# Optimization experiments

Hardware: AMD Instinct MI355X
Metric: run time of the kernel (lower is better)

The kernel has to match this reference:

```python
import jax, jax.numpy as jnp
import numpy as np

EMBED_DIM = 2048
NUM_HEADS = 16
HEAD_DIM = EMBED_DIM // NUM_HEADS  # 128
D_K = 128
SCALE = 1.0 / float(np.sqrt(HEAD_DIM))
LAYER_DEPTH = 6 / 12  # amrpa_layer_idx / n_amrpa_layers
BATCH, SEQ = 2, 2048


def setup_inputs() -> dict:
    key = jax.random.key(0)
    ks = jax.random.split(key, 8)
    return {
        "hidden_states": jax.random.normal(ks[0], (BATCH, SEQ, EMBED_DIM), jnp.float32),
        "c_attn_w": jax.random.normal(ks[1], (EMBED_DIM, 3 * EMBED_DIM), jnp.float32) * 0.02,
        "c_attn_b": jax.random.normal(ks[2], (3 * EMBED_DIM,), jnp.float32) * 0.02,
        "c_proj_w": jax.random.normal(ks[3], (EMBED_DIM, EMBED_DIM), jnp.float32) * 0.02,
        "c_proj_b": jax.random.normal(ks[4], (EMBED_DIM,), jnp.float32) * 0.02,
        "cam_gate": jax.random.normal(ks[5], (D_K,), jnp.float32) * 0.1,
        "cam_w0": jax.random.normal(ks[6], (1,), jnp.float32),
        "cam_w1": jax.random.normal(ks[7], (1,), jnp.float32),
    }


def reference(hidden_states, c_attn_w, c_attn_b, c_proj_w, c_proj_b, cam_gate, cam_w0, cam_w1):
    # GPT2 Conv1D-style fused QKV projection: [B,S,3E]
    qkv = hidden_states @ c_attn_w + c_attn_b
    Q, K, V = jnp.split(qkv, 3, axis=2)  # each [B,S,E]
    # NOTE: faithful to source — attention over the FULL embed dim (no head split),
    # scaled by 1/sqrt(head_dim); causal mask is computed but never applied upstream.
    attn_scores = jnp.einsum('bse,bte->bst', Q, K) * SCALE  # [B,S,S]

    # CAM: sliced low-rank channels
    Q_cam, K_cam, V_cam = Q[:, :, :D_K], K[:, :, :D_K], V[:, :, :D_K]
    # base attention map computed under no_grad in the original
    base_A = jax.lax.stop_gradient(
        jax.nn.softmax(jnp.einsum('bsd,btd->bst', Q_cam, K_cam) * SCALE, axis=-1))
    layer_weight = jax.nn.sigmoid(cam_w0[0] + cam_w1[0] * LAYER_DEPTH)
    cam_ctx = jnp.einsum('bst,btd->bsd', base_A, V_cam)            # [B,S,d_k]
    cam_bias = jnp.einsum('bsd,btd->bst', jnp.tanh(cam_ctx * cam_gate), K_cam)
    cam_bias = cam_bias * (SCALE * layer_weight)                   # cam_mask is all-ones

    final_attn = jax.nn.softmax(attn_scores + cam_bias, axis=-1)
    context = jnp.einsum('bst,bte->bse', final_attn, V)            # [B,S,E]
    output = context @ c_proj_w + c_proj_b                         # resid_dropout is identity (eval)
    return output
```

## Files before the change

### kernel.cpp

```cpp
#include <hip/hip_runtime.h>
#include <hip/hip_bf16.h>

typedef unsigned short u16;
typedef __attribute__((ext_vector_type(8))) __bf16 bf16x8;
typedef __attribute__((ext_vector_type(4))) float f32x4;
typedef __attribute__((ext_vector_type(4))) unsigned short u16x4;

#define SCALE_QK 0.08838834764831845f

__device__ __forceinline__ u16 f2bf(float x) {
  union { float f; unsigned u; } v; v.f = x;
  unsigned r = v.u + 0x7fffu + ((v.u >> 16) & 1u);
  return (u16)(r >> 16);
}

__device__ __forceinline__ void gload_lds16(const u16* g, u16* l) {
  __builtin_amdgcn_global_load_lds(
      (const __attribute__((address_space(1))) unsigned*)g,
      (__attribute__((address_space(3))) unsigned*)l, 16, 0, 0);
}

#define CFENCE() asm volatile("" ::: "memory")
#define WAITV(N) asm volatile("s_waitcnt vmcnt(" #N ")" ::: "memory")

template<bool OUT_BF16, bool HAS_BIAS, bool TWO_SEG>
__global__ __launch_bounds__(512, 2)
void g128d(const u16* __restrict__ A1, int lda1, long sA1,
           const u16* __restrict__ B1, int ldb1, long sB1, int K1,
           const u16* __restrict__ A2, int lda2, long sA2,
           const u16* __restrict__ B2, int ldb2, long sB2, int K2,
           void* __restrict__ Cv, int ldc, long sC,
           float scale, const float* __restrict__ bias, int nbx)
{
  extern __shared__ u16 lds[];
  const int bz = blockIdx.z;
  const int nwg = gridDim.x, orig = blockIdx.x;
  const int q8 = nwg >> 3, r8 = nwg & 7;
  const int xcd = orig & 7, lp = orig >> 3;
  const int wg = (xcd < r8 ? xcd * (q8 + 1) : r8 * (q8 + 1) + (xcd - r8) * q8) + lp;
  const int bx = wg % nbx, by = wg / nbx;
  const long m0 = (long)by * 256, n0 = (long)bx * 128;

  const int tid = threadIdx.x, wid = tid >> 6, lane = tid & 63;
  const int wm = wid >> 1, wn = wid & 1;
  const int rl = lane & 15, g = lane >> 4;
  const int sw = ((g ^ ((rl >> 1) & 3)) << 3);

  int aoff[4], boff[4];
#pragma unroll
  for (int i = 0; i < 4; ++i) aoff[i] = (wm * 64 + i * 16 + rl) * 32 + sw;
#pragma unroll
  for (int j = 0; j < 4; ++j) boff[j] = (wn * 64 + j * 16 + rl) * 32 + sw;

  const int srow = tid >> 2;
  const int scolX = (((tid & 3) ^ ((srow >> 1) & 3)) << 3);

  f32x4 acc[4][4];
#pragma unroll
  for (int i = 0; i < 4; ++i)
#pragma unroll
    for (int j = 0; j < 4; ++j) acc[i][j] = (f32x4){0.f, 0.f, 0.f, 0.f};

  bf16x8 avA[4], bvA[4], avB[4], bvB[4];

#define STG6(H_, OA_) {                                                  \
    const u16* sa_ = Ab + (long)srow * lda + (H_) * 32 + scolX;          \
    u16* da_ = lds + (OA_) + tid * 8;                                    \
    gload_lds16(sa_, da_);                                               \
    gload_lds16(sa_ + (long)128 * lda, da_ + 4096);                      \
    gload_lds16(Bb + (long)srow * ldb + (H_) * 32 + scolX,               \
                lds + 49152 + ((OA_) >> 1) + tid * 8); }
#define RD6(OA_, AV, BV) {                                               \
    const u16* ap_ = lds + (OA_);                                        \
    const u16* bp_ = lds + 49152 + ((OA_) >> 1);                         \
    _Pragma("unroll") for (int i_ = 0; i_ < 4; ++i_)                     \
      AV[i_] = *(const bf16x8*)(ap_ + aoff[i_]);                         \
    _Pragma("unroll") for (int j_ = 0; j_ < 4; ++j_)                     \
      BV[j_] = *(const bf16x8*)(bp_ + boff[j_]); }
#define MMCL(CAV, CBV)                                                   \
    CFENCE(); __builtin_amdgcn_s_barrier();                              \
    asm volatile("s_waitcnt lgkmcnt(0)" ::: "memory");                   \
    __builtin_amdgcn_sched_barrier(0);                                   \
    __builtin_amdgcn_s_setprio(1);                                       \
    _Pragma("unroll") for (int i_ = 0; i_ < 4; ++i_)                     \
      _Pragma("unroll") for (int j_ = 0; j_ < 4; ++j_)                   \
        acc[i_][j_] = __builtin_amdgcn_mfma_f32_16x16x32_bf16(           \
            CAV[i_], CBV[j_], acc[i_][j_], 0, 0, 0);                     \
    __builtin_amdgcn_s_setprio(0);

  const int NSEG = TWO_SEG ? 2 : 1;
#pragma unroll 1
  for (int seg = 0; seg < NSEG; ++seg) {
    const int lda = (seg == 0) ? lda1 : lda2;
    const int ldb = (seg == 0) ? ldb1 : ldb2;
    const int K   = (seg == 0) ? K1 : K2;
    const u16* Ab = ((seg == 0) ? A1 + (long)bz * sA1 : A2 + (long)bz * sA2) + m0 * (long)lda;
    const u16* Bb = ((seg == 0) ? B1 + (long)bz * sB1 : B2 + (long)bz * sB2) + n0 * (long)ldb;
    const int NT = K >> 5;

    if (NT == 4) {
      STG6(0, 0); STG6(1, 8192); STG6(2, 16384); STG6(3, 24576);
      WAITV(9);
      CFENCE(); __builtin_amdgcn_s_barrier(); CFENCE();
      RD6(0, avA, bvA);
      CFENCE();
      WAITV(6); MMCL(avA, bvA); RD6(8192,  avB, bvB); CFENCE();
      WAITV(3); MMCL(avB, bvB); RD6(16384, avA, bvA); CFENCE();
      WAITV(0); MMCL(avA, bvA); RD6(24576, avB, bvB); CFENCE();
      MMCL(avB, bvB); CFENCE();
      __builtin_amdgcn_s_barrier();
      CFENCE();
    } else {
      STG6(0, 0); STG6(1, 8192); STG6(2, 16384); STG6(3, 24576); STG6(4, 32768);
      WAITV(12);
      CFENCE(); __builtin_amdgcn_s_barrier(); CFENCE();
      RD6(0, avA, bvA);
      STG6(5, 40960);
      CFENCE();

      int rdo = 8192;
      int sto = 0;
      int hst = 6;

#pragma unroll 1
      for (int k = 0; k < NT - 6; k += 2) {
        WAITV(12);
        MMCL(avA, bvA);
        RD6(rdo, avB, bvB); rdo += 8192; if (rdo == 49152) rdo = 0;
        STG6(hst, sto); ++hst; sto += 8192; if (sto == 49152) sto = 0;
        CFENCE();
        WAITV(12);
        MMCL(avB, bvB);
        RD6(rdo, avA, bvA); rdo += 8192; if (rdo == 49152) rdo = 0;
        STG6(hst, sto); ++hst; sto += 8192; if (sto == 49152) sto = 0;
        CFENCE();
      }
      WAITV(12); MMCL(avA, bvA);
      RD6(rdo, avB, bvB); rdo += 8192; if (rdo == 49152) rdo = 0; CFENCE();
      WAITV(9);  MMCL(avB, bvB);
      RD6(rdo, avA, bvA); rdo += 8192; if (rdo == 49152) rdo = 0; CFENCE();
      WAITV(6);  MMCL(avA, bvA);
      RD6(rdo, avB, bvB); rdo += 8192; if (rdo == 49152) rdo = 0; CFENCE();
      WAITV(3);  MMCL(avB, bvB);
      RD6(rdo, avA, bvA); rdo += 8192; if (rdo == 49152) rdo = 0; CFENCE();
      WAITV(0);  MMCL(avA, bvA);
      RD6(rdo, avB, bvB); CFENCE();
      MMCL(avB, bvB); CFENCE();
      __builtin_amdgcn_s_barrier();
      CFENCE();
    }
  }
#undef STG6
#undef RD6
#undef MMCL

  const int r0 = (lane >> 4) << 2;
  const int cL = lane & 15;
#pragma unroll
  for (int i = 0; i < 4; ++i) {
#pragma unroll
    for (int j = 0; j < 4; ++j) {
      const long row = m0 + wm * 64 + i * 16 + r0;
      const long col = n0 + wn * 64 + j * 16 + cL;
      float bvs = 0.f;
      if (HAS_BIAS) bvs = bias[col];
      if (OUT_BF16) {
        u16* Cp = (u16*)Cv + (long)bz * sC;
#pragma unroll
        for (int r = 0; r < 4; ++r)
          Cp[(row + r) * ldc + col] = f2bf(acc[i][j][r] * scale + bvs);
      } else {
        float* Cp = (float*)Cv + (long)bz * sC;
#pragma unroll
        for (int r = 0; r < 4; ++r)
          Cp[(row + r) * ldc + col] = acc[i][j][r] * scale + bvs;
      }
    }
  }
}

template<bool OUT_BF16, bool HAS_BIAS>
__global__ __launch_bounds__(256)
void gemm_bt(const u16* __restrict__ A, int lda, long sA,
             const u16* __restrict__ B, int ldb, long sB,
             void* __restrict__ Cv, int ldc, long sC,
             int K, float scale, const float* __restrict__ bias)
{
  __shared__ u16 As[128 * 64];
  __shared__ u16 Bs[128 * 64];
  const int bz   = blockIdx.z;
  const u16* Ap  = A + (long)bz * sA;
  const u16* Bp  = B + (long)bz * sB;
  const int tid  = threadIdx.x;
  const int wid  = tid >> 6;
  const int lane = tid & 63;
  const long m0  = (long)blockIdx.y * 128;
  const long n0  = (long)blockIdx.x * 128;
  const int lrow = lane >> 3;
  const int lk   = (lane & 7) << 3;
  const int wr   = wid >> 1, wc = wid & 1;

  f32x4 acc[4][4];
#pragma unroll
  for (int i = 0; i < 4; ++i)
#pragma unroll
    for (int j = 0; j < 4; ++j) acc[i][j] = (f32x4){0.f, 0.f, 0.f, 0.f};

  for (int k0 = 0; k0 < K; k0 += 64) {
#pragma unroll
    for (int c4 = 0; c4 < 4; ++c4) {
      const int chunk = (wid << 2) + c4;
      gload_lds16(Ap + (m0 + (chunk << 3) + lrow) * lda + k0 + lk, &As[chunk << 9]);
      gload_lds16(Bp + (n0 + (chunk << 3) + lrow) * ldb + k0 + lk, &Bs[chunk << 9]);
    }
    __syncthreads();
#pragma unroll
    for (int kk = 0; kk < 2; ++kk) {
      bf16x8 af[4], bfr[4];
      const int kof   = (kk << 5) + ((lane >> 4) << 3);
      const int rbase = lane & 15;
#pragma unroll
      for (int i = 0; i < 4; ++i)
        af[i] = *(const bf16x8*)&As[(((wr << 6) + (i << 4) + rbase) << 6) + kof];
#pragma unroll
      for (int j = 0; j < 4; ++j)
        bfr[j] = *(const bf16x8*)&Bs[(((wc << 6) + (j << 4) + rbase) << 6) + kof];
#pragma unroll
      for (int i = 0; i < 4; ++i)
#pragma unroll
        for (int j = 0; j < 4; ++j)
          acc[i][j] = __builtin_amdgcn_mfma_f32_16x16x32_bf16(af[i], bfr[j], acc[i][j], 0, 0, 0);
    }
    __syncthreads();
  }

  const int r0 = (lane >> 4) << 2;
  const int cL = lane & 15;
#pragma unroll
  for (int i = 0; i < 4; ++i) {
#pragma unroll
    for (int j = 0; j < 4; ++j) {
      const long row = m0 + (wr << 6) + (i << 4) + r0;
      const long col = n0 + (wc << 6) + (j << 4) + cL;
      float bv = 0.f;
      if (HAS_BIAS) bv = bias[col];
      if (OUT_BF16) {
        u16* Cp = (u16*)Cv + (long)bz * sC;
#pragma unroll
        for (int r = 0; r < 4; ++r)
          Cp[(row + r) * ldc + col] = f2bf(acc[i][j][r] * scale + bv);
      } else {
        float* Cp = (float*)Cv + (long)bz * sC;
#pragma unroll
        for (int r = 0; r < 4; ++r)
          Cp[(row + r) * ldc + col] = acc[i][j][r] * scale + bv;
      }
    }
  }
}

__global__ __launch_bounds__(256)
void gemm_bt_splitk(const u16* __restrict__ A, int lda, long sA,
                    const u16* __restrict__ B, int ldb, long sB,
                    float* __restrict__ C, int ldc, long sC,
                    int Kslice, float scale)
{
  __shared__ u16 As[128 * 64];
  __shared__ u16 Bs[128 * 64];
  const int ks = blockIdx.z & 7;
  const int bz = blockIdx.z >> 3;
  const u16* Ap  = A + (long)bz * sA + ks * Kslice;
  const u16* Bp  = B + (long)bz * sB + ks * Kslice;
  const int tid  = threadIdx.x;
  const int wid  = tid >> 6;
  const int lane = tid & 63;
  const long m0  = (long)blockIdx.y * 128;
  const long n0  = (long)blockIdx.x * 128;
  const int lrow = lane >> 3;
  const int lk   = (lane & 7) << 3;
  const int wr   = wid >> 1, wc = wid & 1;

  f32x4 acc[4][4];
#pragma unroll
  for (int i = 0; i < 4; ++i)
#pragma unroll
    for (int j = 0; j < 4; ++j) acc[i][j] = (f32x4){0.f, 0.f, 0.f, 0.f};

  for (int k0 = 0; k0 < Kslice; k0 += 64) {
#pragma unroll
    for (int c4 = 0; c4 < 4; ++c4) {
      const int chunk = (wid << 2) + c4;
      gload_lds16(Ap + (m0 + (chunk << 3) + lrow) * lda + k0 + lk, &As[chunk << 9]);
      gload_lds16(Bp + (n0 + (chunk << 3) + lrow) * ldb + k0 + lk, &Bs[chunk << 9]);
    }
    __syncthreads();
#pragma unroll
    for (int kk = 0; kk < 2; ++kk) {
      bf16x8 af[4], bfr[4];
      const int kof   = (kk << 5) + ((lane >> 4) << 3);
      const int rbase = lane & 15;
#pragma unroll
      for (int i = 0; i < 4; ++i)
        af[i] = *(const bf16x8*)&As[(((wr << 6) + (i << 4) + rbase) << 6) + kof];
#pragma unroll
      for (int j = 0; j < 4; ++j)
        bfr[j] = *(const bf16x8*)&Bs[(((wc << 6) + (j << 4) + rbase) << 6) + kof];
#pragma unroll
      for (int i = 0; i < 4; ++i)
#pragma unroll
        for (int j = 0; j < 4; ++j)
          acc[i][j] = __builtin_amdgcn_mfma_f32_16x16x32_bf16(af[i], bfr[j], acc[i][j], 0, 0, 0);
    }
    __syncthreads();
  }

  const int r0 = (lane >> 4) << 2;
  const int cL = lane & 15;
  float* Cp = C + (long)bz * sC;
#pragma unroll
  for (int i = 0; i < 4; ++i) {
#pragma unroll
    for (int j = 0; j < 4; ++j) {
      const long row = m0 + (wr << 6) + (i << 4) + r0;
      const long col = n0 + (wc << 6) + (j << 4) + cL;
#pragma unroll
      for (int r = 0; r < 4; ++r)
        atomicAdd(&Cp[(row + r) * ldc + col], acc[i][j][r] * scale);
    }
  }
}

__global__ __launch_bounds__(256)
void softmax_rows2048(const float* __restrict__ src, u16* __restrict__ dst) {
  const long row = blockIdx.x;
  const float4* s = (const float4*)(src + row * 2048);
  const int tid = threadIdx.x;
  float4 a = s[tid * 2], b = s[tid * 2 + 1];
  float m = fmaxf(fmaxf(fmaxf(a.x, a.y), fmaxf(a.z, a.w)),
                  fmaxf(fmaxf(b.x, b.y), fmaxf(b.z, b.w)));
#pragma unroll
  for (int o = 32; o > 0; o >>= 1) m = fmaxf(m, __shfl_xor(m, o));
  __shared__ float redm[4];
  __shared__ float reds[4];
  if ((tid & 63) == 0) redm[tid >> 6] = m;
  __syncthreads();
  m = fmaxf(fmaxf(redm[0], redm[1]), fmaxf(redm[2], redm[3]));
  float e[8];
  e[0] = __expf(a.x - m); e[1] = __expf(a.y - m); e[2] = __expf(a.z - m); e[3] = __expf(a.w - m);
  e[4] = __expf(b.x - m); e[5] = __expf(b.y - m); e[6] = __expf(b.z - m); e[7] = __expf(b.w - m);
  float sum = e[0] + e[1] + e[2] + e[3] + e[4] + e[5] + e[6] + e[7];
#pragma unroll
  for (int o = 32; o > 0; o >>= 1) sum += __shfl_xor(sum, o);
  if ((tid & 63) == 0) reds[tid >> 6] = sum;
  __syncthreads();
  sum = reds[0] + reds[1] + reds[2] + reds[3];
  const float inv = 1.f / sum;
  u16x4 o1 = { f2bf(e[0] * inv), f2bf(e[1] * inv), f2bf(e[2] * inv), f2bf(e[3] * inv) };
  u16x4 o2 = { f2bf(e[4] * inv), f2bf(e[5] * inv), f2bf(e[6] * inv), f2bf(e[7] * inv) };
  u16x4* d = (u16x4*)(dst + row * 2048);
  d[tid * 2]     = o1;
  d[tid * 2 + 1] = o2;
}

__global__ void transpose_f32_to_bf16(const float* __restrict__ src, u16* __restrict__ dst,
                                      int R, int C) {
  __shared__ float t[32][33];
  const int c0 = blockIdx.x * 32, r0 = blockIdx.y * 32;
  const int tx = threadIdx.x, ty = threadIdx.y;
#pragma unroll
  for (int i = 0; i < 4; ++i)
    t[ty + i * 8][tx] = src[(long)(r0 + ty + i * 8) * C + c0 + tx];
  __syncthreads();
#pragma unroll
  for (int i = 0; i < 4; ++i)
    dst[(long)(c0 + ty + i * 8) * R + r0 + tx] = f2bf(t[tx][ty + i * 8]);
}

__global__ void transpose_bf16_batched(const u16* __restrict__ src, int ss, long sbat,
                                       u16* __restrict__ dst, int ds, long dbat) {
  __shared__ u16 t[32][33];
  const u16* s = src + (long)blockIdx.z * sbat;
  u16* d = dst + (long)blockIdx.z * dbat;
  const int c0 = blockIdx.x * 32, r0 = blockIdx.y * 32;
  const int tx = threadIdx.x, ty = threadIdx.y;
#pragma unroll
  for (int i = 0; i < 4; ++i)
    t[ty + i * 8][tx] = s[(long)(r0 + ty + i * 8) * ss + c0 + tx];
  __syncthreads();
#pragma unroll
  for (int i = 0; i < 4; ++i)
    d[(long)(c0 + ty + i * 8) * ds + r0 + tx] = t[tx][ty + i * 8];
}

__global__ __launch_bounds__(256)
void convert_f32_to_bf16(const float* __restrict__ src, u16* __restrict__ dst, long n4) {
  long i = (long)blockIdx.x * 256 + threadIdx.x;
  if (i < n4) {
    float4 v = ((const float4*)src)[i];
    *(u16x4*)(dst + i * 4) = (u16x4){ f2bf(v.x), f2bf(v.y), f2bf(v.z), f2bf(v.w) };
  }
}

__global__ __launch_bounds__(256)
void cam_tanh_kernel(const float* __restrict__ ctx, const float* __restrict__ gate,
                     const float* __restrict__ lw, u16* __restrict__ out, int n) {
  int i = blockIdx.x * 256 + threadIdx.x;
  if (i < n) {
    int d = i & 127;
    out[i] = f2bf(tanhf(ctx[i] * gate[d]) * lw[0]);
  }
}

__global__ __launch_bounds__(256)
void zero_f32(float* __restrict__ p, int n) {
  int i = blockIdx.x * 256 + threadIdx.x;
  if (i < n) p[i] = 0.f;
}

__global__ void calc_lw_kernel(const float* w0, const float* w1, float* lw) {
  *lw = 1.f / (1.f + __expf(-(w0[0] + 0.5f * w1[0])));
}

extern "C" void kernel_launch(void* const* d_in, const int* in_sizes, int n_in,
                              void* d_out, int out_size, void* d_ws, size_t ws_size,
                              hipStream_t stream) {
  const float* hs       = (const float*)d_in[0];
  const float* c_attn_w = (const float*)d_in[1];
  const float* c_attn_b = (const float*)d_in[2];
  const float* c_proj_w = (const float*)d_in[3];
  const float* c_proj_b = (const float*)d_in[4];
  const float* cam_gate = (const float*)d_in[5];
  const float* cam_w0   = (const float*)d_in[6];
  const float* cam_w1   = (const float*)d_in[7];
  float* out = (float*)d_out;

  char* w = (char*)d_ws;
  float* lw      = (float*)(w + 0);
  u16*   hs_b    = (u16*)(w + 256);
  u16*   waT_b   = (u16*)(w + 256 + 16777216UL);
  u16*   wpT_b   = (u16*)(w + 256 + 41943040UL);
  u16*   qkv_b   = (u16*)(w + 256 + 50331648UL);
  u16*   vT_b    = (u16*)(w + 256 + 100663296UL);
  float* scoresF = (float*)(w + 256 + 117440512UL);
  float* camS    = (float*)(w + 256 + 150994944UL);
  float* ctxF    = (float*)(w + 256 + 184549376UL);
  u16*   camT_b  = (u16*)(w + 256 + 186646528UL);
  u16* baseA_b = hs_b;
  u16* P_b     = (u16*)camS;
  u16* ctxE_b  = (u16*)scoresF;

  dim3 b256(256);
  const int LDSB = 147456;

  hipFuncSetAttribute((const void*)g128d<true, true, false>,
                      hipFuncAttributeMaxDynamicSharedMemorySize, LDSB);
  hipFuncSetAttribute((const void*)g128d<false, false, true>,
                      hipFuncAttributeMaxDynamicSharedMemorySize, LDSB);
  hipFuncSetAttribute((const void*)g128d<true, false, false>,
                      hipFuncAttributeMaxDynamicSharedMemorySize, LDSB);
  hipFuncSetAttribute((const void*)g128d<false, true, false>,
                      hipFuncAttributeMaxDynamicSharedMemorySize, LDSB);

  calc_lw_kernel<<<dim3(1), dim3(1), 0, stream>>>(cam_w0, cam_w1, lw);
  convert_f32_to_bf16<<<dim3(8192), b256, 0, stream>>>(hs, hs_b, 2097152L);
  transpose_f32_to_bf16<<<dim3(192, 64), dim3(32, 8), 0, stream>>>(c_attn_w, waT_b, 2048, 6144);
  transpose_f32_to_bf16<<<dim3(64, 64), dim3(32, 8), 0, stream>>>(c_proj_w, wpT_b, 2048, 2048);

  g128d<true, true, false><<<dim3(768, 1, 1), dim3(512), LDSB, stream>>>(
      hs_b, 2048, 0L, waT_b, 2048, 0L, 2048,
      nullptr, 0, 0L, nullptr, 0, 0L, 0,
      qkv_b, 6144, 0L, 1.f, c_attn_b, 48);

  transpose_bf16_batched<<<dim3(64, 64, 2), dim3(32, 8), 0, stream>>>(
      qkv_b + 4096, 6144, 2048L * 6144, vT_b, 2048, 2048L * 2048);

  gemm_bt<false, false><<<dim3(16, 16, 2), b256, 0, stream>>>(
      qkv_b, 6144, 2048L * 6144, qkv_b + 2048, 6144, 2048L * 6144,
      camS, 2048, 2048L * 2048, 128, SCALE_QK, nullptr);

  softmax_rows2048<<<dim3(4096), b256, 0, stream>>>(camS, baseA_b);

  zero_f32<<<dim3(2048), b256, 0, stream>>>(ctxF, 524288);
  gemm_bt_splitk<<<dim3(1, 16, 16), b256, 0, stream>>>(
      baseA_b, 2048, 2048L * 2048, vT_b, 2048, 2048L * 2048,
      ctxF, 128, 2048L * 128, 256, 1.f);

  cam_tanh_kernel<<<dim3(2048), b256, 0, stream>>>(ctxF, cam_gate, lw, camT_b, 524288);

  g128d<false, false, true><<<dim3(128, 1, 2), dim3(512), LDSB, stream>>>(
      qkv_b, 6144, 2048L * 6144, qkv_b + 2048, 6144, 2048L * 6144, 2048,
      camT_b, 128, 2048L * 128, qkv_b + 2048, 6144, 2048L * 6144, 128,
      scoresF, 2048, 2048L * 2048, SCALE_QK, nullptr, 16);

  softmax_rows2048<<<dim3(4096), b256, 0, stream>>>(scoresF, P_b);

  g128d<true, false, false><<<dim3(128, 1, 2), dim3(512), LDSB, stream>>>(
      P_b, 2048, 2048L * 2048, vT_b, 2048, 2048L * 2048, 2048,
      nullptr, 0, 0L, nullptr, 0, 0L, 0,
      ctxE_b, 2048, 2048L * 2048, 1.f, nullptr, 16);

  g128d<false, true, false><<<dim3(256, 1, 1), dim3(512), LDSB, stream>>>(
      ctxE_b, 2048, 0L, wpT_b, 2048, 0L, 2048,
      nullptr, 0, 0L, nullptr, 0, 0L, 0,
      out, 2048, 0L, 1.f, c_proj_b, 16);
}
```

Baseline: 353.0 us.

## Fuse V transpose into QKV GEMM epilogue and drop auxiliary kernels

The QKV projection epilogue now writes the V columns directly in transposed layout into vT_b, which removes the separate batched transpose kernel. A new block mapping groups QKV tiles into rectangles for better L2 reuse. The small CAM score GEMM now uses the g128d kernel instead of the older gemm_bt, and the layer-weight sigmoid is computed inline in cam_tanh, removing two launches. The transposed 4-element stores are strided, and V is no longer written to qkv_b (nothing reads it there).

```diff
diff --git a/kernel.cpp b/kernel.cpp
--- a/kernel.cpp
+++ b/kernel.cpp
@@ -30,7 +30,8 @@
            const u16* __restrict__ A2, int lda2, long sA2,
            const u16* __restrict__ B2, int ldb2, long sB2, int K2,
            void* __restrict__ Cv, int ldc, long sC,
-           float scale, const float* __restrict__ bias, int nbx)
+           float scale, const float* __restrict__ bias, int nbx,
+           int mapmode, u16* __restrict__ vTout)
 {
   extern __shared__ u16 lds[];
   const int bz = blockIdx.z;
@@ -38,7 +39,15 @@
   const int q8 = nwg >> 3, r8 = nwg & 7;
   const int xcd = orig & 7, lp = orig >> 3;
   const int wg = (xcd < r8 ? xcd * (q8 + 1) : r8 * (q8 + 1) + (xcd - r8) * q8) + lp;
-  const int bx = wg % nbx, by = wg / nbx;
+  int bx, by;
+  if (mapmode == 1) {
+    const int x = wg / 96, c = wg % 96;
+    const int rect = c / 48, i6 = c % 48;
+    by = rect * 8 + (i6 & 7);
+    bx = x * 6 + (i6 >> 3);
+  } else {
+    by = wg / nbx; bx = wg % nbx;
+  }
   const long m0 = (long)by * 256, n0 = (long)bx * 128;
 
   const int tid = threadIdx.x, wid = tid >> 6, lane = tid & 63;
@@ -166,94 +175,21 @@
       if (HAS_BIAS) bvs = bias[col];
       if (OUT_BF16) {
         u16* Cp = (u16*)Cv + (long)bz * sC;
-#pragma unroll
-        for (int r = 0; r < 4; ++r)
-          Cp[(row + r) * ldc + col] = f2bf(acc[i][j][r] * scale + bvs);
+        if (vTout && col >= 4096) {
+          u16x4 t;
+#pragma unroll
+          for (int r = 0; r < 4; ++r) t[r] = f2bf(acc[i][j][r] * scale + bvs);
+          *(u16x4*)(vTout + ((long)(row >> 11) * 2048 + (col - 4096)) * 2048 + (row & 2047)) = t;
+        } else {
+#pragma unroll
+          for (int r = 0; r < 4; ++r)
+            Cp[(row + r) * ldc + col] = f2bf(acc[i][j][r] * scale + bvs);
+        }
       } else {
         float* Cp = (float*)Cv + (long)bz * sC;
 #pragma unroll
         for (int r = 0; r < 4; ++r)
           Cp[(row + r) * ldc + col] = acc[i][j][r] * scale + bvs;
-      }
-    }
-  }
-}
-
-template<bool OUT_BF16, bool HAS_BIAS>
-__global__ __launch_bounds__(256)
-void gemm_bt(const u16* __restrict__ A, int lda, long sA,
-             const u16* __restrict__ B, int ldb, long sB,
-             void* __restrict__ Cv, int ldc, long sC,
-             int K, float scale, const float* __restrict__ bias)
-{
-  __shared__ u16 As[128 * 64];
-  __shared__ u16 Bs[128 * 64];
-  const int bz   = blockIdx.z;
-  const u16* Ap  = A + (long)bz * sA;
-  const u16* Bp  = B + (long)bz * sB;
-  const int tid  = threadIdx.x;
-  const int wid  = tid >> 6;
-  const int lane = tid & 63;
-  const long m0  = (long)blockIdx.y * 128;
-  const long n0  = (long)blockIdx.x * 128;
-  const int lrow = lane >> 3;
-  const int lk   = (lane & 7) << 3;
-  const int wr   = wid >> 1, wc = wid & 1;
-
-  f32x4 acc[4][4];
-#pragma unroll
-  for (int i = 0; i < 4; ++i)
-#pragma unroll
-    for (int j = 0; j < 4; ++j) acc[i][j] = (f32x4){0.f, 0.f, 0.f, 0.f};
-
-  for (int k0 = 0; k0 < K; k0 += 64) {
-#pragma unroll
-    for (int c4 = 0; c4 < 4; ++c4) {
-      const int chunk = (wid << 2) + c4;
-      gload_lds16(Ap + (m0 + (chunk << 3) + lrow) * lda + k0 + lk, &As[chunk << 9]);
-      gload_lds16(Bp + (n0 + (chunk << 3) + lrow) * ldb + k0 + lk, &Bs[chunk << 9]);
-    }
-    __syncthreads();
-#pragma unroll
-    for (int kk = 0; kk < 2; ++kk) {
-      bf16x8 af[4], bfr[4];
-      const int kof   = (kk << 5) + ((lane >> 4) << 3);
-      const int rbase = lane & 15;
-#pragma unroll
-      for (int i = 0; i < 4; ++i)
-        af[i] = *(const bf16x8*)&As[(((wr << 6) + (i << 4) + rbase) << 6) + kof];
-#pragma unroll
-      for (int j = 0; j < 4; ++j)
-        bfr[j] = *(const bf16x8*)&Bs[(((wc << 6) + (j << 4) + rbase) << 6) + kof];
-#pragma unroll
-      for (int i = 0; i < 4; ++i)
-#pragma unroll
-        for (int j = 0; j < 4; ++j)
-          acc[i][j] = __builtin_amdgcn_mfma_f32_16x16x32_bf16(af[i], bfr[j], acc[i][j], 0, 0, 0);
-    }
-    __syncthreads();
-  }
-
-  const int r0 = (lane >> 4) << 2;
-  const int cL = lane & 15;
-#pragma unroll
-  for (int i = 0; i < 4; ++i) {
-#pragma unroll
-    for (int j = 0; j < 4; ++j) {
-      const long row = m0 + (wr << 6) + (i << 4) + r0;
-      const long col = n0 + (wc << 6) + (j << 4) + cL;
-      float bv = 0.f;
-      if (HAS_BIAS) bv = bias[col];
-      if (OUT_BF16) {
-        u16* Cp = (u16*)Cv + (long)bz * sC;
-#pragma unroll
-        for (int r = 0; r < 4; ++r)
-          Cp[(row + r) * ldc + col] = f2bf(acc[i][j][r] * scale + bv);
-      } else {
-        float* Cp = (float*)Cv + (long)bz * sC;
-#pragma unroll
-        for (int r = 0; r < 4; ++r)
-          Cp[(row + r) * ldc + col] = acc[i][j][r] * scale + bv;
       }
     }
   }
@@ -376,22 +312,6 @@
     dst[(long)(c0 + ty + i * 8) * R + r0 + tx] = f2bf(t[tx][ty + i * 8]);
 }
 
-__global__ void transpose_bf16_batched(const u16* __restrict__ src, int ss, long sbat,
-                                       u16* __restrict__ dst, int ds, long dbat) {
-  __shared__ u16 t[32][33];
-  const u16* s = src + (long)blockIdx.z * sbat;
-  u16* d = dst + (long)blockIdx.z * dbat;
-  const int c0 = blockIdx.x * 32, r0 = blockIdx.y * 32;
-  const int tx = threadIdx.x, ty = threadIdx.y;
-#pragma unroll
-  for (int i = 0; i < 4; ++i)
-    t[ty + i * 8][tx] = s[(long)(r0 + ty + i * 8) * ss + c0 + tx];
-  __syncthreads();
-#pragma unroll
-  for (int i = 0; i < 4; ++i)
-    d[(long)(c0 + ty + i * 8) * ds + r0 + tx] = t[tx][ty + i * 8];
-}
-
 __global__ __launch_bounds__(256)
 void convert_f32_to_bf16(const float* __restrict__ src, u16* __restrict__ dst, long n4) {
   long i = (long)blockIdx.x * 256 + threadIdx.x;
@@ -403,11 +323,13 @@
 
 __global__ __launch_bounds__(256)
 void cam_tanh_kernel(const float* __restrict__ ctx, const float* __restrict__ gate,
-                     const float* __restrict__ lw, u16* __restrict__ out, int n) {
+                     const float* __restrict__ w0, const float* __restrict__ w1,
+                     u16* __restrict__ out, int n) {
   int i = blockIdx.x * 256 + threadIdx.x;
   if (i < n) {
+    const float lw = 1.f / (1.f + __expf(-(w0[0] + 0.5f * w1[0])));
     int d = i & 127;
-    out[i] = f2bf(tanhf(ctx[i] * gate[d]) * lw[0]);
+    out[i] = f2bf(tanhf(ctx[i] * gate[d]) * lw);
   }
 }
 
@@ -415,10 +337,6 @@
 void zero_f32(float* __restrict__ p, int n) {
   int i = blockIdx.x * 256 + threadIdx.x;
   if (i < n) p[i] = 0.f;
-}
-
-__global__ void calc_lw_kernel(const float* w0, const float* w1, float* lw) {
-  *lw = 1.f / (1.f + __expf(-(w0[0] + 0.5f * w1[0])));
 }
 
 extern "C" void kernel_launch(void* const* d_in, const int* in_sizes, int n_in,
@@ -435,7 +353,6 @@
   float* out = (float*)d_out;
 
   char* w = (char*)d_ws;
-  float* lw      = (float*)(w + 0);
   u16*   hs_b    = (u16*)(w + 256);
   u16*   waT_b   = (u16*)(w + 256 + 16777216UL);
   u16*   wpT_b   = (u16*)(w + 256 + 41943040UL);
@@ -454,6 +371,8 @@
 
   hipFuncSetAttribute((const void*)g128d<true, true, false>,
                       hipFuncAttributeMaxDynamicSharedMemorySize, LDSB);
+  hipFuncSetAttribute((const void*)g128d<false, false, false>,
+                      hipFuncAttributeMaxDynamicSharedMemorySize, LDSB);
   hipFuncSetAttribute((const void*)g128d<false, false, true>,
                       hipFuncAttributeMaxDynamicSharedMemorySize, LDSB);
   hipFuncSetAttribute((const void*)g128d<true, false, false>,
@@ -461,7 +380,6 @@
   hipFuncSetAttribute((const void*)g128d<false, true, false>,
                       hipFuncAttributeMaxDynamicSharedMemorySize, LDSB);
 
-  calc_lw_kernel<<<dim3(1), dim3(1), 0, stream>>>(cam_w0, cam_w1, lw);
   convert_f32_to_bf16<<<dim3(8192), b256, 0, stream>>>(hs, hs_b, 2097152L);
   transpose_f32_to_bf16<<<dim3(192, 64), dim3(32, 8), 0, stream>>>(c_attn_w, waT_b, 2048, 6144);
   transpose_f32_to_bf16<<<dim3(64, 64), dim3(32, 8), 0, stream>>>(c_proj_w, wpT_b, 2048, 2048);
@@ -469,14 +387,12 @@
   g128d<true, true, false><<<dim3(768, 1, 1), dim3(512), LDSB, stream>>>(
       hs_b, 2048, 0L, waT_b, 2048, 0L, 2048,
       nullptr, 0, 0L, nullptr, 0, 0L, 0,
-      qkv_b, 6144, 0L, 1.f, c_attn_b, 48);
-
-  transpose_bf16_batched<<<dim3(64, 64, 2), dim3(32, 8), 0, stream>>>(
-      qkv_b + 4096, 6144, 2048L * 6144, vT_b, 2048, 2048L * 2048);
-
-  gemm_bt<false, false><<<dim3(16, 16, 2), b256, 0, stream>>>(
-      qkv_b, 6144, 2048L * 6144, qkv_b + 2048, 6144, 2048L * 6144,
-      camS, 2048, 2048L * 2048, 128, SCALE_QK, nullptr);
+      qkv_b, 6144, 0L, 1.f, c_attn_b, 48, 1, vT_b);
+
+  g128d<false, false, false><<<dim3(128, 1, 2), dim3(512), LDSB, stream>>>(
+      qkv_b, 6144, 2048L * 6144, qkv_b + 2048, 6144, 2048L * 6144, 128,
+      nullptr, 0, 0L, nullptr, 0, 0L, 0,
+      camS, 2048, 2048L * 2048, SCALE_QK, nullptr, 16, 0, nullptr);
 
   softmax_rows2048<<<dim3(4096), b256, 0, stream>>>(camS, baseA_b);
 
@@ -485,22 +401,23 @@
       baseA_b, 2048, 2048L * 2048, vT_b, 2048, 2048L * 2048,
       ctxF, 128, 2048L * 128, 256, 1.f);
 
-  cam_tanh_kernel<<<dim3(2048), b256, 0, stream>>>(ctxF, cam_gate, lw, camT_b, 524288);
+  cam_tanh_kernel<<<dim3(2048), b256, 0, stream>>>(ctxF, cam_gate, cam_w0, cam_w1,
+                                                   camT_b, 524288);
 
   g128d<false, false, true><<<dim3(128, 1, 2), dim3(512), LDSB, stream>>>(
       qkv_b, 6144, 2048L * 6144, qkv_b + 2048, 6144, 2048L * 6144, 2048,
       camT_b, 128, 2048L * 128, qkv_b + 2048, 6144, 2048L * 6144, 128,
-      scoresF, 2048, 2048L * 2048, SCALE_QK, nullptr, 16);
+      scoresF, 2048, 2048L * 2048, SCALE_QK, nullptr, 16, 0, nullptr);
 
   softmax_rows2048<<<dim3(4096), b256, 0, stream>>>(scoresF, P_b);
 
   g128d<true, false, false><<<dim3(128, 1, 2), dim3(512), LDSB, stream>>>(
       P_b, 2048, 2048L * 2048, vT_b, 2048, 2048L * 2048, 2048,
       nullptr, 0, 0L, nullptr, 0, 0L, 0,
-      ctxE_b, 2048, 2048L * 2048, 1.f, nullptr, 16);
+      ctxE_b, 2048, 2048L * 2048, 1.f, nullptr, 16, 0, nullptr);
 
   g128d<false, true, false><<<dim3(256, 1, 1), dim3(512), LDSB, stream>>>(
       ctxE_b, 2048, 0L, wpT_b, 2048, 0L, 2048,
       nullptr, 0, 0L, nullptr, 0, 0L, 0,
-      out, 2048, 0L, 1.f, c_proj_b, 16);
-}
+      out, 2048, 0L, 1.f, c_proj_b, 16, 0, nullptr);
+}
```

Result: faster. 345.0 us (-2.3%).
